# Kernel tuning notes

Hardware: AMD Instinct MI355X
Metric: run time of the kernel (lower is better)

## Reference

```python
import jax, jax.numpy as jnp
import numpy as np

NUM_GROUPS = 8
EPS = 1e-5


def setup_inputs() -> dict:
    key = jax.random.key(0)
    ks = jax.random.split(key, 7)
    b, c, h, w = 4, 256, 64, 64
    x = jax.random.normal(ks[0], (b, c, h, w), dtype=jnp.float32)
    gamma = jnp.ones((c,), dtype=jnp.float32)
    beta = jnp.zeros((c,), dtype=jnp.float32)
    # 1x1 convs stored as [out_ch, in_ch] matrices
    w_qkv = jax.random.normal(ks[1], (3 * c, c), dtype=jnp.float32) * (1.0 / np.sqrt(c))
    b_qkv = jax.random.normal(ks[2], (3 * c,), dtype=jnp.float32) * 0.01
    # NOTE: original zero-inits proj; use small random weights so the op is non-trivial
    w_proj = jax.random.normal(ks[3], (c, c), dtype=jnp.float32) * (1.0 / np.sqrt(c))
    b_proj = jax.random.normal(ks[4], (c,), dtype=jnp.float32) * 0.01
    return {"x": x, "gamma": gamma, "beta": beta, "w_qkv": w_qkv,
            "b_qkv": b_qkv, "w_proj": w_proj, "b_proj": b_proj}


def _group_norm(x, gamma, beta):
    b, c, h, w = x.shape
    xg = x.reshape(b, NUM_GROUPS, c // NUM_GROUPS, h, w)
    mean = jnp.mean(xg, axis=(2, 3, 4), keepdims=True)
    var = jnp.var(xg, axis=(2, 3, 4), keepdims=True)
    xg = (xg - mean) * jax.lax.rsqrt(var + EPS)
    x = xg.reshape(b, c, h, w)
    return x * gamma[None, :, None, None] + beta[None, :, None, None]


def reference(x, gamma, beta, w_qkv, b_qkv, w_proj, b_proj):
    b, c, h, w = x.shape
    n = h * w
    residual = x
    xn = _group_norm(x, gamma, beta)
    # 1x1 conv qkv: [b, 3c, h, w]
    qkv = jnp.einsum('bchw,oc->bohw', xn, w_qkv) + b_qkv[None, :, None, None]
    q, k, v = jnp.split(qkv, 3, axis=1)
    q = q.reshape(b, c, n).transpose(0, 2, 1)   # [b, n, c]
    k = k.reshape(b, c, n)                       # [b, c, n]
    v = v.reshape(b, c, n).transpose(0, 2, 1)   # [b, n, c]
    scale = 1.0 / jnp.sqrt(jnp.asarray(c, dtype=x.dtype))
    attn = jnp.einsum('bic,bcj->bij', q, k) * scale    # [b, n, n]
    attn = jax.nn.softmax(attn, axis=-1)
    out = jnp.einsum('bij,bjc->bic', attn, v)          # [b, n, c]
    out = out.transpose(0, 2, 1).reshape(b, c, h, w)
    out = jnp.einsum('bchw,oc->bohw', out, w_proj) + b_proj[None, :, None, None]
    return out + residual
```

## Files before the change

kernel.cpp:

```cpp
#include <hip/hip_runtime.h>
#include <math.h>

#define BB   4
#define CC   256
#define NN   4096
#define GG   8
#define CPG  32
#define EPSV 1e-5f
#define SCALE 0.0625f
#define NSPLIT 4
#define PSTR 40

typedef __attribute__((ext_vector_type(8))) short bf16x8;
typedef __attribute__((ext_vector_type(4))) float f32x4;

struct alignas(8) us4 { unsigned short x, y, z, w; };

static __device__ __forceinline__ unsigned short f2bf(float f) {
    union { float f; unsigned int u; } a; a.f = f;
    unsigned int r = a.u + 0x7fffu + ((a.u >> 16) & 1u);
    return (unsigned short)(r >> 16);
}
static __device__ __forceinline__ void async16(const unsigned short* g, unsigned short* l) {
    __builtin_amdgcn_global_load_lds(
        (const __attribute__((address_space(1))) unsigned int*)g,
        (__attribute__((address_space(3))) unsigned int*)l,
        16, 0, 0);
}

__global__ __launch_bounds__(256) void prep_kernel(
    const float* __restrict__ x, const float* __restrict__ w_qkv,
    const float* __restrict__ w_proj, float* __restrict__ partials,
    unsigned short* __restrict__ wbf)
{
    const int tid = threadIdx.x;
    if (blockIdx.x >= 256) {
        int idx = ((blockIdx.x - 256)*256 + tid) * 4;
        float4 v;
        if (idx < 196608) v = *(const float4*)(w_qkv + idx);
        else              v = *(const float4*)(w_proj + (idx - 196608));
        us4 h = { f2bf(v.x), f2bf(v.y), f2bf(v.z), f2bf(v.w) };
        *(us4*)(wbf + idx) = h;
        return;
    }
    const int bg = blockIdx.x >> 3, slice = blockIdx.x & 7;
    const float4* base = (const float4*)(x + (size_t)bg*CPG*NN + slice*16384);
    float s = 0.f, sq = 0.f;
    for (int i = tid; i < 4096; i += 256) {
        float4 v = base[i];
        s  += v.x + v.y + v.z + v.w;
        sq += v.x*v.x + v.y*v.y + v.z*v.z + v.w*v.w;
    }
    __shared__ float ls[256], lq[256];
    ls[tid] = s; lq[tid] = sq;
    __syncthreads();
    for (int off = 128; off > 0; off >>= 1) {
        if (tid < off) { ls[tid] += ls[tid+off]; lq[tid] += lq[tid+off]; }
        __syncthreads();
    }
    if (tid == 0) { partials[blockIdx.x*2] = ls[0]; partials[blockIdx.x*2+1] = lq[0]; }
}

__global__ __launch_bounds__(256) void norm_t_kernel(
    const float* __restrict__ x, const float* __restrict__ gamma,
    const float* __restrict__ beta, const float* __restrict__ partials,
    unsigned short* __restrict__ xnT)
{
    const int n0 = blockIdx.x * 64;
    const int c0 = blockIdx.y * 64;
    const int b  = blockIdx.z;
    const int tid = threadIdx.x;
    __shared__ unsigned short T[64*68];
    __shared__ float ssc[64], ssh[64];
    if (tid < 64) {
        int c = c0 + tid;
        int bg = b*GG + (c >> 5);
        float s = 0.f, sq = 0.f;
        for (int i = 0; i < 8; i++) {
            s  += partials[(bg*8 + i)*2];
            sq += partials[(bg*8 + i)*2 + 1];
        }
        const float cnt = (float)(CPG*NN);
        float mean = s / cnt;
        float var  = sq / cnt - mean*mean;
        float rstd = rsqrtf(var + EPSV);
        float g = gamma[c], be = beta[c];
        ssc[tid] = rstd*g;
        ssh[tid] = be - mean*rstd*g;
    }
    __syncthreads();
    {
        int cl = tid >> 4, n4 = tid & 15;
        for (int i = 0; i < 4; i++) {
            int c = cl + i*16;
            float4 v = *(const float4*)(x + ((size_t)(b*CC + c0 + c))*NN + n0 + n4*4);
            float sc = ssc[c], sh = ssh[c];
            T[(n4*4+0)*68 + c] = f2bf(v.x*sc + sh);
            T[(n4*4+1)*68 + c] = f2bf(v.y*sc + sh);
            T[(n4*4+2)*68 + c] = f2bf(v.z*sc + sh);
            T[(n4*4+3)*68 + c] = f2bf(v.w*sc + sh);
        }
    }
    __syncthreads();
    {
        int nl = tid >> 3, cs = tid & 7;
        for (int i = 0; i < 2; i++) {
            int n = nl + i*32;
            *(bf16x8*)(xnT + ((size_t)(b*NN + n0 + n))*CC + c0 + cs*8) =
                *(const bf16x8*)&T[n*68 + cs*8];
        }
    }
}

__global__ __launch_bounds__(256) void qkv_mfma_kernel(
    const unsigned short* __restrict__ xnT, const unsigned short* __restrict__ wbf,
    const float* __restrict__ b_qkv,
    unsigned short* __restrict__ qsw, unsigned short* __restrict__ ksw,
    unsigned short* __restrict__ vsw)
{
    const int tid  = threadIdx.x;
    const int wave = tid >> 6, lane = tid & 63;
    const int lrow = lane & 15, quad = lane >> 4;
    const int R0   = blockIdx.x * 128;
    const int b    = blockIdx.x >> 5;
    const int nb0  = (blockIdx.x & 31) * 128;
    const int oBase = blockIdx.y * 64;
    const int which = oBase >> 8;
    const int o0l   = oBase & 255;
    const bool isV  = (which == 2);
    const int wn = wave >> 1, wo = wave & 1;

    const unsigned short* Abase;
    const unsigned short* Bbase;
    if (!isV) {
        Abase = wbf + ((size_t)(oBase + lrow))*CC + quad*8;
        Bbase = xnT + ((size_t)(R0 + wave*32 + lrow))*CC + quad*8;
    } else {
        Abase = xnT + ((size_t)(R0 + wn*64 + lrow))*CC + quad*8;
        Bbase = wbf + ((size_t)(oBase + wo*32 + lrow))*CC + quad*8;
    }

    f32x4 acc[4][2];
    for (int s = 0; s < 4; s++) for (int t = 0; t < 2; t++)
        acc[s][t] = (f32x4){0.f, 0.f, 0.f, 0.f};

    for (int c0 = 0; c0 < CC; c0 += 32) {
        bf16x8 af[4], bfr[2];
        for (int s = 0; s < 4; s++) af[s]  = *(const bf16x8*)(Abase + s*16*CC + c0);
        for (int t = 0; t < 2; t++) bfr[t] = *(const bf16x8*)(Bbase + t*16*CC + c0);
        for (int s = 0; s < 4; s++)
            for (int t = 0; t < 2; t++)
                acc[s][t] = __builtin_amdgcn_mfma_f32_16x16x32_bf16(af[s], bfr[t], acc[s][t], 0, 0, 0);
    }

    __shared__ unsigned short lds[8192];

    if (!isV) {
        const float sc = (which == 0) ? SCALE : 1.0f;
        for (int s = 0; s < 4; s++) {
            float bias[4];
            for (int r = 0; r < 4; r++) bias[r] = b_qkv[oBase + s*16 + quad*4 + r];
            for (int t = 0; t < 2; t++) {
                us4 h;
                h.x = f2bf((acc[s][t][0] + bias[0]) * sc);
                h.y = f2bf((acc[s][t][1] + bias[1]) * sc);
                h.z = f2bf((acc[s][t][2] + bias[2]) * sc);
                h.w = f2bf((acc[s][t][3] + bias[3]) * sc);
                int chunk = (wave*2 + t)*2 + (s>>1);
                int pos = (((s*2 + (quad>>1)) & 3)*16 + lrow)*8 + (quad&1)*4;
                *(us4*)&lds[chunk*512 + pos] = h;
            }
        }
    } else {
        for (int s = 0; s < 4; s++)
            for (int t = 0; t < 2; t++) {
                int oc = o0l + wo*32 + t*16 + lrow;
                float bias = b_qkv[512 + oc];
                us4 h;
                h.x = f2bf(acc[s][t][0] + bias);
                h.y = f2bf(acc[s][t][1] + bias);
                h.z = f2bf(acc[s][t][2] + bias);
                h.w = f2bf(acc[s][t][3] + bias);
                int chunk = (wn*2 + (s>>1))*4 + wo*2 + t;
                int pos = (((s&1)*2 + (quad>>1))*16 + lrow)*8 + (quad&1)*4;
                *(us4*)&lds[chunk*512 + pos] = h;
            }
    }
    __syncthreads();

    if (!isV) {
        unsigned short* dst = (which == 0) ? qsw : ksw;
        for (int it = 0; it < 4; it++) {
            int f = it*4 + (tid>>6);
            int ng_l = f >> 1, kk_l = f & 1;
            size_t off = ((size_t)(b*256 + (nb0>>4) + ng_l)*8 + (o0l>>5) + kk_l)*512 + lane*8;
            *(bf16x8*)(dst + off) = *(const bf16x8*)&lds[f*512 + lane*8];
        }
    } else {
        for (int it = 0; it < 4; it++) {
            int f = it*4 + (tid>>6);
            int jg_l = f >> 2, ns_l = f & 3;
            size_t off = ((size_t)(b*128 + (nb0>>5) + jg_l)*16 + (o0l>>4) + ns_l)*512 + lane*8;
            *(bf16x8*)(vsw + off) = *(const bf16x8*)&lds[f*512 + lane*8];
        }
    }
}

__global__ __launch_bounds__(256, 2) void attn_mfma_kernel(
    const unsigned short* __restrict__ qsw, const unsigned short* __restrict__ ksw,
    const unsigned short* __restrict__ vsw,
    unsigned short* __restrict__ opart, float* __restrict__ lpart)
{
    const int tid  = threadIdx.x;
    const int wave = tid >> 6, lane = tid & 63;
    const int lrow = lane & 15, quad = lane >> 4;
    const int bx    = blockIdx.x;
    const int split = bx & 3;
    const int ig    = (bx >> 2) & 31;
    const int b     = bx >> 7;
    const int i0w   = ig*128 + wave*32;
    const int koff  = split * (NN / NSPLIT);
    const int NT    = (NN / NSPLIT) / 32;

    __shared__ unsigned short ldsK[2][8192];
    __shared__ unsigned short ldsV[2][8192];
    __shared__ unsigned short ldsP[4][32*PSTR];

    bf16x8 qf[2][8];
    {
        const unsigned short* qb = qsw + ((size_t)b << 20) + (size_t)i0w*256 + lane*8;
        for (int g = 0; g < 2; g++)
            for (int kk = 0; kk < 8; kk++)
                qf[g][kk] = *(const bf16x8*)(qb + g*4096 + kk*512);
    }

    f32x4 o_acc[2][16];
    for (int g = 0; g < 2; g++)
        for (int ns = 0; ns < 16; ns++)
            o_acc[g][ns] = (f32x4){0.f, 0.f, 0.f, 0.f};
    float lsum[2] = {0.f, 0.f};

    const unsigned short* kp = ksw + ((size_t)b << 20) + (size_t)koff*256 + wave*2048 + lane*8;
    const unsigned short* vp = vsw + ((size_t)b << 20) + (size_t)koff*256 + wave*2048 + lane*8;

    for (int t = 0; t < 4; t++) {
        async16(kp + t*512, ldsK[0] + wave*2048 + t*512);
        async16(vp + t*512, ldsV[0] + wave*2048 + t*512);
    }
    asm volatile("s_waitcnt vmcnt(0)" ::: "memory");
    __builtin_amdgcn_s_barrier();

    for (int jt = 0; jt < NT; jt++) {
        const int cur = jt & 1, nxt = cur ^ 1;

        if (jt + 1 < NT) {
            for (int t = 0; t < 4; t++) {
                async16(kp + (size_t)(jt+1)*8192 + t*512, ldsK[nxt] + wave*2048 + t*512);
                async16(vp + (size_t)(jt+1)*8192 + t*512, ldsV[nxt] + wave*2048 + t*512);
            }
        }

        f32x4 s[2][2];
        for (int jg = 0; jg < 2; jg++)
            for (int g = 0; g < 2; g++)
                s[jg][g] = (f32x4){0.f, 0.f, 0.f, 0.f};
        const unsigned short* lk = ldsK[cur];
        __builtin_amdgcn_s_setprio(1);
        for (int jg = 0; jg < 2; jg++)
            for (int kk = 0; kk < 8; kk++) {
                bf16x8 kf = *(const bf16x8*)(lk + (jg*8 + kk)*512 + lane*8);
                s[jg][0] = __builtin_amdgcn_mfma_f32_16x16x32_bf16(kf, qf[0][kk], s[jg][0], 0, 0, 0);
                s[jg][1] = __builtin_amdgcn_mfma_f32_16x16x32_bf16(kf, qf[1][kk], s[jg][1], 0, 0, 0);
            }
        __builtin_amdgcn_s_setprio(0);

        unsigned short* pw = ldsP[wave];
        for (int jg = 0; jg < 2; jg++)
            for (int g = 0; g < 2; g++) {
                float p0 = __expf(s[jg][g][0]);
                float p1 = __expf(s[jg][g][1]);
                float p2 = __expf(s[jg][g][2]);
                float p3 = __expf(s[jg][g][3]);
                lsum[g] += p0 + p1 + p2 + p3;
                us4 h = { f2bf(p0), f2bf(p1), f2bf(p2), f2bf(p3) };
                *(us4*)(pw + (g*16 + lrow)*PSTR + jg*16 + quad*4) = h;
            }

        bf16x8 pa[2];
        for (int g = 0; g < 2; g++)
            pa[g] = *(const bf16x8*)(pw + (g*16 + lrow)*PSTR + quad*8);

        const unsigned short* lv = ldsV[cur];
        __builtin_amdgcn_s_setprio(1);
        for (int ns = 0; ns < 16; ns++) {
            bf16x8 vf = *(const bf16x8*)(lv + ns*512 + lane*8);
            o_acc[0][ns] = __builtin_amdgcn_mfma_f32_16x16x32_bf16(pa[0], vf, o_acc[0][ns], 0, 0, 0);
            o_acc[1][ns] = __builtin_amdgcn_mfma_f32_16x16x32_bf16(pa[1], vf, o_acc[1][ns], 0, 0, 0);
        }
        __builtin_amdgcn_s_setprio(0);

        asm volatile("s_waitcnt vmcnt(0) lgkmcnt(0)" ::: "memory");
        __builtin_amdgcn_s_barrier();
    }

    for (int g = 0; g < 2; g++) {
        float v = lsum[g];
        v += __shfl_xor(v, 16);
        v += __shfl_xor(v, 32);
        lsum[g] = v;
    }

    unsigned short* reg = &ldsV[0][0] + wave*4096;
    const size_t planeb = ((size_t)(split*BB + b)) << 20;
    for (int g = 0; g < 2; g++) {
        for (int ns = 0; ns < 16; ns++) {
            int kk = ns >> 1;
            int posbase = ((ns & 1)*2 + (lrow >> 3))*128 + (lrow & 7) + quad*32;
            for (int r = 0; r < 4; r++)
                reg[kk*512 + posbase + r*8] = f2bf(o_acc[g][ns][r]);
        }
        unsigned short* dst = opart + planeb + ((size_t)((i0w >> 4) + g))*4096;
        for (int kk = 0; kk < 8; kk++)
            *(bf16x8*)(dst + kk*512 + lane*8) = *(const bf16x8*)(reg + kk*512 + lane*8);
    }
    if (quad == 0)
        for (int g = 0; g < 2; g++)
            lpart[(size_t)(split*BB + b)*NN + i0w + g*16 + lrow] = lsum[g];
}

__global__ __launch_bounds__(256, 4) void proj_mfma_kernel(
    const unsigned short* __restrict__ opart, const float* __restrict__ lpart,
    const unsigned short* __restrict__ w2bf, const float* __restrict__ b_proj,
    const float* __restrict__ x, float* __restrict__ out)
{
    const int tid  = threadIdx.x;
    const int wave = tid >> 6, lane = tid & 63;
    const int lrow = lane & 15, quad = lane >> 4;
    const int rt = blockIdx.x & 255;
    const int oq = blockIdx.x >> 8;
    const int b  = rt >> 6;
    const int n0 = (rt & 63) * 64;

    const int rg = (n0 >> 4) + wave;
    const unsigned short* Ab = opart + ((size_t)b << 20) + (size_t)rg*4096 + lane*8;
    const size_t pstride = (size_t)BB << 20;

    f32x4 acc[4];
    for (int t = 0; t < 4; t++) acc[t] = (f32x4){0.f, 0.f, 0.f, 0.f};

    for (int kk = 0; kk < 8; kk++) {
        bf16x8 bfr[4];
        for (int t = 0; t < 4; t++)
            bfr[t] = *(const bf16x8*)(w2bf +
                ((size_t)(oq*64 + t*16 + lrow))*CC + kk*32 + quad*8);
        for (int sp = 0; sp < NSPLIT; sp++) {
            bf16x8 af = *(const bf16x8*)(Ab + (size_t)sp*pstride + kk*512);
            for (int t = 0; t < 4; t++)
                acc[t] = __builtin_amdgcn_mfma_f32_16x16x32_bf16(af, bfr[t], acc[t], 0, 0, 0);
        }
    }

    float sinv[4];
    for (int r = 0; r < 4; r++) {
        int n = n0 + wave*16 + quad*4 + r;
        float l = 0.f;
        for (int sp = 0; sp < NSPLIT; sp++)
            l += lpart[(size_t)(sp*BB + b)*NN + n];
        sinv[r] = 1.0f / l;
    }

    for (int t = 0; t < 4; t++) {
        int o = oq*64 + t*16 + lrow;
        int n = n0 + wave*16 + quad*4;
        size_t idx = ((size_t)(b*CC + o))*NN + n;
        float bias = b_proj[o];
        float4 xv = *(const float4*)(x + idx);
        float4 ov;
        ov.x = acc[t][0]*sinv[0] + bias + xv.x;
        ov.y = acc[t][1]*sinv[1] + bias + xv.y;
        ov.z = acc[t][2]*sinv[2] + bias + xv.z;
        ov.w = acc[t][3]*sinv[3] + bias + xv.w;
        *(float4*)(out + idx) = ov;
    }
}

extern "C" void kernel_launch(void* const* d_in, const int* in_sizes, int n_in,
                              void* d_out, int out_size, void* d_ws, size_t ws_size,
                              hipStream_t stream) {
    const float* x      = (const float*)d_in[0];
    const float* gamma  = (const float*)d_in[1];
    const float* beta   = (const float*)d_in[2];
    const float* w_qkv  = (const float*)d_in[3];
    const float* b_qkv  = (const float*)d_in[4];
    const float* w_proj = (const float*)d_in[5];
    const float* b_proj = (const float*)d_in[6];
    float* out = (float*)d_out;

    const size_t plane = (size_t)BB * NN * CC;
    unsigned short* xnT = (unsigned short*)d_ws;
    unsigned short* qsw = xnT + plane;
    unsigned short* ksw = qsw + plane;
    unsigned short* vsw = ksw + plane;
    unsigned short* wbf = vsw + plane;
    unsigned short* opart = wbf + 262144;
    float* lpart    = (float*)(opart + (size_t)NSPLIT*plane);
    float* partials = lpart + (size_t)NSPLIT*BB*NN;

    prep_kernel<<<512, 256, 0, stream>>>(x, w_qkv, w_proj, partials, wbf);

    dim3 gnt(64, 4, BB);
    norm_t_kernel<<<gnt, 256, 0, stream>>>(x, gamma, beta, partials, xnT);

    dim3 gq(128, 12);
    qkv_mfma_kernel<<<gq, 256, 0, stream>>>(xnT, wbf, b_qkv, qsw, ksw, vsw);

    attn_mfma_kernel<<<BB*32*NSPLIT, 256, 0, stream>>>(qsw, ksw, vsw, opart, lpart);

    proj_mfma_kernel<<<1024, 256, 0, stream>>>(opart, lpart, wbf + 196608, b_proj, x, out);
}
```

Before: 220.2 us.

## Pre-swizzle weights and xn into MFMA fragment layout and stage via async LDS loads

```diff
diff --git a/kernel.cpp b/kernel.cpp
--- a/kernel.cpp
+++ b/kernel.cpp
@@ -27,6 +27,7 @@
         (__attribute__((address_space(3))) unsigned int*)l,
         16, 0, 0);
 }
+
 
 __global__ __launch_bounds__(256) void prep_kernel(
     const float* __restrict__ x, const float* __restrict__ w_qkv,
@@ -40,7 +41,10 @@
         if (idx < 196608) v = *(const float4*)(w_qkv + idx);
         else              v = *(const float4*)(w_proj + (idx - 196608));
         us4 h = { f2bf(v.x), f2bf(v.y), f2bf(v.z), f2bf(v.w) };
-        *(us4*)(wbf + idx) = h;
+        int o = idx >> 8, c = idx & 255;
+        size_t dst = ((size_t)((o >> 4)*8 + (c >> 5)))*512
+                   + ((((c & 31) >> 3))*16 + (o & 15))*8 + (c & 7);
+        *(us4*)(wbf + dst) = h;
         return;
     }
     const int bg = blockIdx.x >> 3, slice = blockIdx.x & 7;
@@ -106,13 +110,15 @@
         int nl = tid >> 3, cs = tid & 7;
         for (int i = 0; i < 2; i++) {
             int n = nl + i*32;
-            *(bf16x8*)(xnT + ((size_t)(b*NN + n0 + n))*CC + c0 + cs*8) =
-                *(const bf16x8*)&T[n*68 + cs*8];
-        }
-    }
-}
-
-__global__ __launch_bounds__(256) void qkv_mfma_kernel(
+            int gg = (b*NN + n0 + n) >> 4;
+            int kk = (c0 >> 5) + (cs >> 2);
+            size_t dst = ((size_t)(gg*8 + kk))*512 + ((cs & 3)*16 + (n & 15))*8;
+            *(bf16x8*)(xnT + dst) = *(const bf16x8*)&T[n*68 + cs*8];
+        }
+    }
+}
+
+__global__ __launch_bounds__(256, 3) void qkv_mfma_kernel(
     const unsigned short* __restrict__ xnT, const unsigned short* __restrict__ wbf,
     const float* __restrict__ b_qkv,
     unsigned short* __restrict__ qsw, unsigned short* __restrict__ ksw,
@@ -129,31 +135,56 @@
     const int o0l   = oBase & 255;
     const bool isV  = (which == 2);
     const int wn = wave >> 1, wo = wave & 1;
-
-    const unsigned short* Abase;
-    const unsigned short* Bbase;
-    if (!isV) {
-        Abase = wbf + ((size_t)(oBase + lrow))*CC + quad*8;
-        Bbase = xnT + ((size_t)(R0 + wave*32 + lrow))*CC + quad*8;
-    } else {
-        Abase = xnT + ((size_t)(R0 + wn*64 + lrow))*CC + quad*8;
-        Bbase = wbf + ((size_t)(oBase + wo*32 + lrow))*CC + quad*8;
-    }
+    const int wg0 = oBase >> 4;
+
+    __shared__ unsigned short lw[16384];
+    __shared__ unsigned short lx[2][4096];
+
+    const unsigned short* wsrc = wbf + ((size_t)(wg0 + wave))*8*512 + lane*8;
+    for (int kk = 0; kk < 8; kk++)
+        async16(wsrc + kk*512, lw + (wave*8 + kk)*512);
+    const unsigned short* xsrc = xnT + (size_t)R0*CC + lane*8;
+    for (int i = 0; i < 2; i++) {
+        int g = wave*2 + i;
+        async16(xsrc + (size_t)g*4096, lx[0] + g*512);
+    }
+    asm volatile("s_waitcnt vmcnt(0)" ::: "memory");
+    __builtin_amdgcn_s_barrier();
 
     f32x4 acc[4][2];
     for (int s = 0; s < 4; s++) for (int t = 0; t < 2; t++)
         acc[s][t] = (f32x4){0.f, 0.f, 0.f, 0.f};
 
-    for (int c0 = 0; c0 < CC; c0 += 32) {
+    for (int kk = 0; kk < 8; kk++) {
+        const int cur = kk & 1, nxt = cur ^ 1;
+        if (kk + 1 < 8) {
+            for (int i = 0; i < 2; i++) {
+                int g = wave*2 + i;
+                async16(xsrc + (size_t)g*4096 + (kk+1)*512, lx[nxt] + g*512);
+            }
+        }
         bf16x8 af[4], bfr[2];
-        for (int s = 0; s < 4; s++) af[s]  = *(const bf16x8*)(Abase + s*16*CC + c0);
-        for (int t = 0; t < 2; t++) bfr[t] = *(const bf16x8*)(Bbase + t*16*CC + c0);
+        if (!isV) {
+            for (int s = 0; s < 4; s++)
+                af[s]  = *(const bf16x8*)(lw + (s*8 + kk)*512 + lane*8);
+            for (int t = 0; t < 2; t++)
+                bfr[t] = *(const bf16x8*)(lx[cur] + (wave*2 + t)*512 + lane*8);
+        } else {
+            for (int s = 0; s < 4; s++)
+                af[s]  = *(const bf16x8*)(lx[cur] + (wn*4 + s)*512 + lane*8);
+            for (int t = 0; t < 2; t++)
+                bfr[t] = *(const bf16x8*)(lw + ((wo*2 + t)*8 + kk)*512 + lane*8);
+        }
+        __builtin_amdgcn_s_setprio(1);
         for (int s = 0; s < 4; s++)
             for (int t = 0; t < 2; t++)
                 acc[s][t] = __builtin_amdgcn_mfma_f32_16x16x32_bf16(af[s], bfr[t], acc[s][t], 0, 0, 0);
-    }
-
-    __shared__ unsigned short lds[8192];
+        __builtin_amdgcn_s_setprio(0);
+        asm volatile("s_waitcnt vmcnt(0) lgkmcnt(0)" ::: "memory");
+        __builtin_amdgcn_s_barrier();
+    }
+
+    unsigned short* lds = lw;
 
     if (!isV) {
         const float sc = (which == 0) ? SCALE : 1.0f;
@@ -345,19 +376,34 @@
     const unsigned short* Ab = opart + ((size_t)b << 20) + (size_t)rg*4096 + lane*8;
     const size_t pstride = (size_t)BB << 20;
 
+    __shared__ unsigned short la[2][8192];
+
+    for (int sp = 0; sp < NSPLIT; sp++)
+        async16(Ab + (size_t)sp*pstride, la[0] + (wave*4 + sp)*512);
+    asm volatile("s_waitcnt vmcnt(0)" ::: "memory");
+
     f32x4 acc[4];
     for (int t = 0; t < 4; t++) acc[t] = (f32x4){0.f, 0.f, 0.f, 0.f};
 
     for (int kk = 0; kk < 8; kk++) {
+        const int cur = kk & 1, nxt = cur ^ 1;
+        if (kk + 1 < 8)
+            for (int sp = 0; sp < NSPLIT; sp++)
+                async16(Ab + (size_t)sp*pstride + (kk+1)*512, la[nxt] + (wave*4 + sp)*512);
+
         bf16x8 bfr[4];
         for (int t = 0; t < 4; t++)
-            bfr[t] = *(const bf16x8*)(w2bf +
-                ((size_t)(oq*64 + t*16 + lrow))*CC + kk*32 + quad*8);
+            bfr[t] = *(const bf16x8*)(w2bf + ((size_t)((oq*4 + t)*8 + kk))*512 + lane*8);
+
+        __builtin_amdgcn_s_setprio(1);
         for (int sp = 0; sp < NSPLIT; sp++) {
-            bf16x8 af = *(const bf16x8*)(Ab + (size_t)sp*pstride + kk*512);
+            bf16x8 af = *(const bf16x8*)(la[cur] + (wave*4 + sp)*512 + lane*8);
             for (int t = 0; t < 4; t++)
                 acc[t] = __builtin_amdgcn_mfma_f32_16x16x32_bf16(af, bfr[t], acc[t], 0, 0, 0);
         }
+        __builtin_amdgcn_s_setprio(0);
+
+        asm volatile("s_waitcnt vmcnt(0)" ::: "memory");
     }
 
     float sinv[4];
```

After: 190.4 us. 13.5% less time.
